# Kernel tuning notes

Measured on AMD Instinct MI355X. Metric: run time of the kernel, lower is better.

The kernel has to match this reference:

```python
import jax, jax.numpy as jnp
import numpy as np

HEADS, DIM, N = 16, 128, 2048
NEG = -1e9


def setup_inputs() -> dict:
    key = jax.random.key(0)
    ks = jax.random.split(key, 8)
    xavier = lambda k, shape, fan: jax.random.uniform(
        k, shape, jnp.float32, -1.0, 1.0) * np.sqrt(6.0 / fan)
    return {
        "q": jax.random.normal(ks[0], (N, DIM), jnp.float32),
        "k": jax.random.normal(ks[1], (N, DIM), jnp.float32),
        "v": jax.random.normal(ks[2], (N, DIM), jnp.float32),
        "mask": jax.random.randint(ks[3], (N, N), 0, 2) > 0,
        "Q": xavier(ks[4], (HEADS, DIM, DIM), 2 * DIM),
        "K": xavier(ks[5], (HEADS, DIM, DIM), 2 * DIM),
        "V": xavier(ks[6], (HEADS, DIM, DIM), 2 * DIM),
        "last": xavier(ks[7], (HEADS * DIM, DIM), HEADS * DIM + DIM),
    }


def reference(q, k, v, Q, K, V, last, mask):
    # per-head projections: [n, d] x [h, d, d] -> [h, n, d]
    qp = jnp.einsum('nd,hde->hne', q, Q)
    kp = jnp.einsum('nd,hde->hne', k, K)
    vp = jnp.einsum('nd,hde->hne', v, V)
    n = qp.shape[1]
    # NOTE: original computes k @ q^T and scales by sqrt(seq_len) (q.size(1) after projection)
    att = jnp.einsum('hid,hjd->hij', kp, qp)  # [h, n, n]
    fmask = mask.astype(jnp.float32)
    att = att * fmask / jnp.sqrt(jnp.float32(n)) + NEG * (1.0 - fmask)
    att = jax.nn.softmax(att, axis=2)
    out = jnp.einsum('hij,hjd->hid', att, vp)            # [h, n, d]
    out = jnp.transpose(out, (1, 0, 2)).reshape(n, -1)   # n (heads d)
    return out @ last
```

## Files before the change

### kernel.cpp

```cpp
#include <hip/hip_runtime.h>
#include <hip/hip_bf16.h>


#define HN 16
#define NN 2048
#define DD 128

typedef __attribute__((ext_vector_type(8))) short short8;
typedef __attribute__((ext_vector_type(4))) short short4v;
typedef __attribute__((ext_vector_type(4))) float float4v;
typedef __attribute__((ext_vector_type(16))) float f32x16;
typedef __attribute__((ext_vector_type(4))) unsigned int uint4v;

#define CROW(r) ((((r) & 3)) + 8 * ((r) >> 2))

__device__ inline unsigned short f2bf(float f) {
    unsigned int u = __builtin_bit_cast(unsigned int, f);
    unsigned int r = (u + 0x7fffu + ((u >> 16) & 1u)) >> 16;
    return (unsigned short)r;
}

__device__ inline unsigned int cvtpk(float lo, float hi) {
    unsigned int w;
    asm("v_cvt_pk_bf16_f32 %0, %1, %2" : "=v"(w) : "v"(lo), "v"(hi));
    return w;
}

__device__ inline void plswap(unsigned int& x, unsigned int& y) {
#if __has_builtin(__builtin_amdgcn_permlane32_swap)
    typedef int int2v __attribute__((ext_vector_type(2)));
    int2v r = __builtin_amdgcn_permlane32_swap((int)x, (int)y, false, false);
    x = (unsigned int)r[0];
    y = (unsigned int)r[1];
#else
    const unsigned int sx = (unsigned int)__shfl_xor((int)x, 32);
    const unsigned int sy = (unsigned int)__shfl_xor((int)y, 32);
    const bool hiHalf = (threadIdx.x & 32) != 0;
    const unsigned int nx = hiHalf ? sy : x;
    const unsigned int ny = hiHalf ? y : sx;
    x = nx; y = ny;
#endif
}

__device__ inline short8 ld_bf8(const float* __restrict__ p) {
    const float4v a = *(const float4v*)p;
    const float4v b = *(const float4v*)(p + 4);
    short8 r;
    r[0] = (short)f2bf(a[0]); r[1] = (short)f2bf(a[1]);
    r[2] = (short)f2bf(a[2]); r[3] = (short)f2bf(a[3]);
    r[4] = (short)f2bf(b[0]); r[5] = (short)f2bf(b[1]);
    r[6] = (short)f2bf(b[2]); r[7] = (short)f2bf(b[3]);
    return r;
}

__device__ inline short8 ld2x4(const unsigned short* p) {
    const short4v lo = *(const short4v*)p;
    const short4v hi = *(const short4v*)(p + 4);
    short8 r;
    r[0] = lo[0]; r[1] = lo[1]; r[2] = lo[2]; r[3] = lo[3];
    r[4] = hi[0]; r[5] = hi[1]; r[6] = hi[2]; r[7] = hi[3];
    return r;
}

__global__ void sentinel_kernel(float* out, int n) {
    int i = blockIdx.x * 256 + threadIdx.x;
    if (i < n) out[i] = 2.0f;
}

__global__ __launch_bounds__(256) void prep_kernel(
    const int* __restrict__ mask,
    unsigned long long* __restrict__ mbT,
    float* __restrict__ out, int out_n,
    const float* __restrict__ Qw,
    const float* __restrict__ Kw,
    const float* __restrict__ Vw,
    unsigned short* __restrict__ wsW)
{
    __shared__ __align__(16) unsigned short Wt[128 * 132];
    const int bx = blockIdx.x;
    const int tid = threadIdx.x;

    if (bx < 4096) {
        const int wgrp = bx * 4 + (tid >> 6);
        const int lane = tid & 63;
        const int word0 = wgrp * 4;
        const int i = word0 >> 5;
        const int w = word0 & 31;
        const int* row = mask + (size_t)i * NN + w * 64;
        unsigned long long b[4];
#pragma unroll
        for (int c = 0; c < 4; c++)
            b[c] = __ballot(row[c * 64 + lane] != 0);
        if (lane == 0) {
#pragma unroll
            for (int c = 0; c < 4; c++) mbT[(size_t)(w + c) * NN + i] = b[c];
        }
        const int z = bx * 256 + tid;
        if (z < out_n) out[z] = 0.f;
    } else {
        const int idx = bx - 4096;
        const int h = idx & 15, t = idx >> 4;
        const float* W = ((t == 0) ? Qw : ((t == 1) ? Kw : Vw)) + h * DD * DD;
        unsigned short* o = wsW + ((size_t)t * HN + h) * DD * DD;

        for (int idx2 = tid * 2; idx2 < DD * DD; idx2 += 512) {
            const int d = idx2 >> 7, e = idx2 & 127;
            const float2 w2 = *(const float2*)(W + idx2);
            Wt[(e + 0) * 132 + d] = f2bf(w2.x);
            Wt[(e + 1) * 132 + d] = f2bf(w2.y);
        }
        __syncthreads();
        for (int idx8 = tid * 8; idx8 < DD * DD; idx8 += 2048) {
            const int e = idx8 >> 7, d = idx8 & 127;
            *(short8*)(o + idx8) = ld2x4(&Wt[e * 132 + d]);
        }
    }
}

__global__ __launch_bounds__(256) void proj4_kernel(
    const float* __restrict__ q,
    const float* __restrict__ k,
    const float* __restrict__ v,
    const unsigned short* __restrict__ wsW,
    unsigned short* __restrict__ ws)
{
    __shared__ __align__(16) unsigned short Wt[128 * 136];
    const int t = blockIdx.z, h = blockIdx.y, cb = blockIdx.x;
    const int tid = threadIdx.x;
    const float* in = (t == 0) ? q : ((t == 1) ? k : v);
    const unsigned short* WTg = wsW + ((size_t)t * HN + h) * DD * DD;
    unsigned short* out = ws + (size_t)t * (HN * NN * DD) + (size_t)h * (NN * DD);

#pragma unroll
    for (int it = 0; it < 8; it++) {
        const int idx8 = tid * 8 + it * 2048;
        const int row = idx8 >> 7, col = idx8 & 127;
        *(short8*)(&Wt[row * 136 + col]) = *(const short8*)(WTg + idx8);
    }
    __syncthreads();

    const int wave = tid >> 6, lane = tid & 63;
    const int quad = lane >> 4, l16 = lane & 15;

#pragma unroll 1
    for (int rt = 0; rt < 2; rt++) {
        const int row0 = cb * 128 + rt * 64 + wave * 16;

        float4v acc[8];
#pragma unroll
        for (int c = 0; c < 8; c++) acc[c] = {0.f, 0.f, 0.f, 0.f};

        if (t < 2) {
#pragma unroll
            for (int kk = 0; kk < 4; kk++) {
                const short8 a = ld_bf8(in + (size_t)(row0 + l16) * DD + kk * 32 + quad * 8);
#pragma unroll
                for (int c = 0; c < 8; c++) {
                    const short8 b = *(const short8*)(&Wt[(c * 16 + l16) * 136 + kk * 32 + quad * 8]);
                    acc[c] = __builtin_amdgcn_mfma_f32_16x16x32_bf16(a, b, acc[c], 0, 0, 0);
                }
            }
            if (t == 0) {
#pragma unroll
                for (int c = 0; c < 8; c++)
#pragma unroll
                    for (int r = 0; r < 4; r++) {
                        const int row = row0 + quad * 4 + r;
                        out[(size_t)(((row >> 5) * 8 + c)) * 512 + (row & 31) * 16 + l16]
                            = f2bf(acc[c][r]);
                    }
            } else {
#pragma unroll
                for (int c = 0; c < 8; c++)
#pragma unroll
                    for (int r = 0; r < 4; r++)
                        out[(size_t)(row0 + quad * 4 + r) * DD + c * 16 + l16] = f2bf(acc[c][r]);
            }
        } else {
#pragma unroll
            for (int kk = 0; kk < 4; kk++) {
                const short8 bv = ld_bf8(in + (size_t)(row0 + l16) * DD + kk * 32 + quad * 8);
#pragma unroll
                for (int c = 0; c < 8; c++) {
                    const short8 aw = *(const short8*)(&Wt[(c * 16 + l16) * 136 + kk * 32 + quad * 8]);
                    acc[c] = __builtin_amdgcn_mfma_f32_16x16x32_bf16(aw, bv, acc[c], 0, 0, 0);
                }
            }
#pragma unroll
            for (int c = 0; c < 8; c++)
#pragma unroll
                for (int r = 0; r < 4; r++) {
                    const int d = c * 16 + quad * 4 + r;
                    out[(size_t)(row0 >> 4) * 2048 + d * 16 + l16] = f2bf(acc[c][r]);
                }
        }
    }
}

__global__ __launch_bounds__(256, 2) void attn_kernel(
    unsigned short* __restrict__ ws,
    const unsigned long long* __restrict__ mbT,
    const float* __restrict__ last,
    float* __restrict__ outp)
{
    __shared__ __align__(16) float obuf[2 * 128 * 33];
    __shared__ __align__(16) unsigned short lastT[128 * 132];
    __shared__ float lbuf[192];

    const int bid = blockIdx.x;
    const int xcd = bid & 7;
    const int h  = xcd + 8 * (bid >> 8);
    const int ib = (bid >> 3) & 31;
    const int tid = threadIdx.x;
    const int wave = tid >> 6, lane = tid & 63;
    const int ig = wave >> 1;
    const int h2 = wave & 1;
    const int l31 = lane & 31;
    const int hi = lane >> 5;

    const unsigned short* qA  = ws + (size_t)h * (NN * DD);
    const unsigned short* kp  = ws + (size_t)(HN * NN * DD) + (size_t)h * (NN * DD);
    const unsigned short* vpB = ws + (size_t)(2 * HN * NN * DD) + (size_t)h * (NN * DD);

    const int i0 = ib * 64;
    const float scale = 0.022097086912079612f;

    {
        const float* lastH = last + (size_t)h * DD * DD;
        for (int idx2 = tid * 2; idx2 < DD * DD; idx2 += 512) {
            const int kk = idx2 >> 7, e = idx2 & 127;
            const float2 w2 = *(const float2*)(lastH + idx2);
            lastT[(e + 0) * 132 + kk] = f2bf(w2.x);
            lastT[(e + 1) * 132 + kk] = f2bf(w2.y);
        }
    }

    short8 kpf[8];
    {
        const int row = i0 + ig * 32 + l31;
#pragma unroll
        for (int kk = 0; kk < 8; kk++)
            kpf[kk] = *(const short8*)(kp + (size_t)row * DD + kk * 16 + hi * 8);
    }

    const unsigned short* qbase = qA + l31 * 16 + hi * 8;
    const unsigned short* vbase = vpB + l31 * 16 + hi * 8;

    f32x16 o[4];
#pragma unroll
    for (int dt = 0; dt < 4; dt++)
#pragma unroll
        for (int r = 0; r < 16; r++) o[dt][r] = 0.f;
    float lacc = 0.f;

    short8 qfA[8], qfB[8];

#define QLD(QF, JT) do {                                                        \
        const unsigned short* p_ = qbase + (size_t)(((JT) * 2 + h2) * 8) * 512; \
        _Pragma("unroll")                                                       \
        for (int kk = 0; kk < 8; kk++)                                          \
            QF[kk] = *(const short8*)(p_ + kk * 512);                           \
    } while (0)

    auto COMPUTE = [&](const short8 (&qf)[8], int jt) {
        short8 vf[8];
#pragma unroll
        for (int ks = 0; ks < 2; ks++)
#pragma unroll
            for (int dt = 0; dt < 4; dt++)
                vf[ks * 4 + dt] = *(const short8*)(vbase
                    + (size_t)(jt * 4 + h2 * 2 + ks) * 2048 + dt * 512);
        const unsigned long long mrow = mbT[(size_t)jt * NN + i0 + ig * 32 + l31];
        const unsigned int m2 = (unsigned int)(mrow >> (h2 * 32 + hi * 4));

        f32x16 s;
#pragma unroll
        for (int r = 0; r < 16; r++) s[r] = 0.f;
        __builtin_amdgcn_s_setprio(1);
#pragma unroll
        for (int kk = 0; kk < 8; kk++)
            s = __builtin_amdgcn_mfma_f32_32x32x16_bf16(qf[kk], kpf[kk], s, 0, 0, 0);
        __builtin_amdgcn_s_setprio(0);

#pragma unroll
        for (int r = 0; r < 16; r++) {
            const float x = ((m2 >> CROW(r)) & 1u) ? fmaf(s[r], scale, -5.0f) : -50.0f;
            s[r] = __expf(x);
        }
        float ls = (((s[0] + s[1]) + (s[2] + s[3])) + ((s[4] + s[5]) + (s[6] + s[7])))
                 + (((s[8] + s[9]) + (s[10] + s[11])) + ((s[12] + s[13]) + (s[14] + s[15])));
        ls += __shfl_xor(ls, 32);
        lacc += ls;

        short8 pa[2];
#pragma unroll
        for (int ks = 0; ks < 2; ks++) {
            const int b = ks * 8;
            unsigned int x0 = cvtpk(s[b + 0], s[b + 1]);
            unsigned int y0 = cvtpk(s[b + 4], s[b + 5]);
            unsigned int x1 = cvtpk(s[b + 2], s[b + 3]);
            unsigned int y1 = cvtpk(s[b + 6], s[b + 7]);
            plswap(x0, y0);
            plswap(x1, y1);
            uint4v w; w[0] = x0; w[1] = x1; w[2] = y0; w[3] = y1;
            pa[ks] = __builtin_bit_cast(short8, w);
        }

        __builtin_amdgcn_s_setprio(1);
#pragma unroll
        for (int ks = 0; ks < 2; ks++)
#pragma unroll
            for (int dt = 0; dt < 4; dt++)
                o[dt] = __builtin_amdgcn_mfma_f32_32x32x16_bf16(pa[ks], vf[ks * 4 + dt], o[dt], 0, 0, 0);
        __builtin_amdgcn_s_setprio(0);
    };

    QLD(qfA, 0);
#pragma unroll 1
    for (int jt = 0; jt < 32; jt += 2) {
        QLD(qfB, jt + 1);
        COMPUTE(qfA, jt);
        if (jt + 2 < 32) QLD(qfA, jt + 2);
        COMPUTE(qfB, jt + 1);
    }
#undef QLD

    if (h2 == 1) {
#pragma unroll
        for (int dt = 0; dt < 4; dt++)
#pragma unroll
            for (int r = 0; r < 16; r++)
                obuf[(size_t)(ig * 128 + dt * 32 + l31) * 33 + CROW(r) + hi * 4] = o[dt][r];
        if (hi == 0) lbuf[ig * 32 + l31] = lacc;
    }
    __syncthreads();

    if (h2 == 0) {
        const float lt = lacc + lbuf[ig * 32 + l31];
        const float inv = (lt > 0.f) ? (1.0f / lt) : 0.f;
        if (hi == 0) lbuf[64 + ig * 32 + l31] = inv;
#pragma unroll
        for (int dt = 0; dt < 4; dt++)
#pragma unroll
            for (int r = 0; r < 16; r++) {
                const int row = CROW(r) + hi * 4;
                const size_t oi = (size_t)(ig * 128 + dt * 32 + l31) * 33 + row;
                obuf[oi] = (o[dt][r] + obuf[oi]) * lbuf[64 + ig * 32 + row];
            }
    }
    __syncthreads();

    short8 af[8];
#pragma unroll
    for (int kk = 0; kk < 8; kk++) {
        const float* ob = &obuf[(size_t)(ig * 128 + kk * 16 + hi * 8) * 33 + l31];
        uint4v w;
        w[0] = cvtpk(ob[0 * 33], ob[1 * 33]);
        w[1] = cvtpk(ob[2 * 33], ob[3 * 33]);
        w[2] = cvtpk(ob[4 * 33], ob[5 * 33]);
        w[3] = cvtpk(ob[6 * 33], ob[7 * 33]);
        af[kk] = __builtin_bit_cast(short8, w);
    }
    f32x16 acc2[2];
#pragma unroll
    for (int ebx = 0; ebx < 2; ebx++)
#pragma unroll
        for (int r = 0; r < 16; r++) acc2[ebx][r] = 0.f;
#pragma unroll
    for (int kk = 0; kk < 8; kk++) {
#pragma unroll
        for (int ebx = 0; ebx < 2; ebx++) {
            const short8 bf = ld2x4(&lastT[(size_t)((h2 * 2 + ebx) * 32 + l31) * 132
                                           + kk * 16 + hi * 8]);
            acc2[ebx] = __builtin_amdgcn_mfma_f32_32x32x16_bf16(af[kk], bf, acc2[ebx], 0, 0, 0);
        }
    }
#pragma unroll
    for (int ebx = 0; ebx < 2; ebx++)
#pragma unroll
        for (int r = 0; r < 16; r++)
            atomicAdd(&outp[(size_t)(i0 + ig * 32 + CROW(r) + 4 * hi) * DD
                            + (h2 * 2 + ebx) * 32 + l31],
                      acc2[ebx][r]);
}

extern "C" void kernel_launch(void* const* d_in, const int* in_sizes, int n_in,
                              void* d_out, int out_size, void* d_ws, size_t ws_size,
                              hipStream_t stream)
{
    const float* q    = (const float*)d_in[0];
    const float* k    = (const float*)d_in[1];
    const float* v    = (const float*)d_in[2];
    const int*   mask = (const int*)d_in[3];
    const float* Qw   = (const float*)d_in[4];
    const float* Kw   = (const float*)d_in[5];
    const float* Vw   = (const float*)d_in[6];
    const float* last = (const float*)d_in[7];
    unsigned short* ws  = (unsigned short*)d_ws;
    float* out = (float*)d_out;

    const size_t shorts_main = (size_t)4 * HN * NN * DD;
    const size_t mb_bytes = (size_t)NN * (NN / 64) * 8;
    const size_t needed = shorts_main * sizeof(unsigned short) + mb_bytes;
    if (ws_size < needed) {
        sentinel_kernel<<<(out_size + 255) / 256, 256, 0, stream>>>(out, out_size);
        return;
    }
    unsigned long long* mbT = (unsigned long long*)(ws + shorts_main);
    unsigned short* wsW = ws + (size_t)3 * HN * NN * DD;

    prep_kernel<<<dim3(4096 + 48), 256, 0, stream>>>(mask, mbT, out, out_size,
                                                     Qw, Kw, Vw, wsW);
    proj4_kernel<<<dim3(16, 16, 3), 256, 0, stream>>>(q, k, v, wsW, ws);
    attn_kernel<<<dim3(512), 256, 0, stream>>>(ws, mbT, last, out);
}
```

Measured before the change: 156.3 us.

## Fuse projection into prep kernel and precompute bf16 output weights

Merges the weight-transpose prep and the per-head Q/K/V projection into one launch: each projection block now converts and transposes its own fp32 weight tile into LDS, so the separate proj kernel and its bf16 weight round trip go away. The mask bit-packing blocks and 16 new blocks that convert the final output weight to bf16 run in the same grid. The attention kernel then loads pre-converted bf16 output weights with vector loads instead of converting fp32 per block. The cost is that each of the 768 projection blocks redoes the fp32 weight conversion, where before it was done once per weight matrix.

```diff
diff --git a/kernel.cpp b/kernel.cpp
--- a/kernel.cpp
+++ b/kernel.cpp
@@ -11,6 +11,7 @@
 typedef __attribute__((ext_vector_type(4))) float float4v;
 typedef __attribute__((ext_vector_type(16))) float f32x16;
 typedef __attribute__((ext_vector_type(4))) unsigned int uint4v;
+typedef __attribute__((ext_vector_type(2))) unsigned int uint2v;
 
 #define CROW(r) ((((r) & 3)) + 8 * ((r) >> 2))
 
@@ -67,21 +68,97 @@
     if (i < n) out[i] = 2.0f;
 }
 
-__global__ __launch_bounds__(256) void prep_kernel(
+__global__ __launch_bounds__(256) void fused_kernel(
+    const float* __restrict__ q,
+    const float* __restrict__ k,
+    const float* __restrict__ v,
     const int* __restrict__ mask,
-    unsigned long long* __restrict__ mbT,
-    float* __restrict__ out, int out_n,
     const float* __restrict__ Qw,
     const float* __restrict__ Kw,
     const float* __restrict__ Vw,
-    unsigned short* __restrict__ wsW)
+    const float* __restrict__ last,
+    unsigned long long* __restrict__ mbT,
+    float* __restrict__ out, int out_n,
+    unsigned short* __restrict__ ws,
+    unsigned short* __restrict__ lastb)
 {
     __shared__ __align__(16) unsigned short Wt[128 * 132];
     const int bx = blockIdx.x;
     const int tid = threadIdx.x;
 
-    if (bx < 4096) {
-        const int wgrp = bx * 4 + (tid >> 6);
+    if (bx < 768) {
+        const int t = bx >> 8, h = (bx >> 4) & 15, cb = bx & 15;
+        const float* in = (t == 0) ? q : ((t == 1) ? k : v);
+        const float* W  = ((t == 0) ? Qw : ((t == 1) ? Kw : Vw)) + h * DD * DD;
+        unsigned short* outp = ws + (size_t)t * (HN * NN * DD) + (size_t)h * (NN * DD);
+
+        for (int idx2 = tid * 2; idx2 < DD * DD; idx2 += 512) {
+            const int d = idx2 >> 7, e = idx2 & 127;
+            const float2 w2 = *(const float2*)(W + idx2);
+            Wt[(e + 0) * 132 + d] = f2bf(w2.x);
+            Wt[(e + 1) * 132 + d] = f2bf(w2.y);
+        }
+        __syncthreads();
+
+        const int wave = tid >> 6, lane = tid & 63;
+        const int quad = lane >> 4, l16 = lane & 15;
+
+#pragma unroll 1
+        for (int rt = 0; rt < 2; rt++) {
+            const int row0 = cb * 128 + rt * 64 + wave * 16;
+
+            float4v acc[8];
+#pragma unroll
+            for (int c = 0; c < 8; c++) acc[c] = {0.f, 0.f, 0.f, 0.f};
+
+            if (t < 2) {
+#pragma unroll
+                for (int kk = 0; kk < 4; kk++) {
+                    const short8 a = ld_bf8(in + (size_t)(row0 + l16) * DD + kk * 32 + quad * 8);
+#pragma unroll
+                    for (int c = 0; c < 8; c++) {
+                        const short8 b = ld2x4(&Wt[(c * 16 + l16) * 132 + kk * 32 + quad * 8]);
+                        acc[c] = __builtin_amdgcn_mfma_f32_16x16x32_bf16(a, b, acc[c], 0, 0, 0);
+                    }
+                }
+                if (t == 0) {
+#pragma unroll
+                    for (int c = 0; c < 8; c++)
+#pragma unroll
+                        for (int r = 0; r < 4; r++) {
+                            const int row = row0 + quad * 4 + r;
+                            outp[(size_t)(((row >> 5) * 8 + c)) * 512 + (row & 31) * 16 + l16]
+                                = f2bf(acc[c][r]);
+                        }
+                } else {
+#pragma unroll
+                    for (int c = 0; c < 8; c++)
+#pragma unroll
+                        for (int r = 0; r < 4; r++)
+                            outp[(size_t)(row0 + quad * 4 + r) * DD + c * 16 + l16] = f2bf(acc[c][r]);
+                }
+            } else {
+#pragma unroll
+                for (int kk = 0; kk < 4; kk++) {
+                    const short8 bv = ld_bf8(in + (size_t)(row0 + l16) * DD + kk * 32 + quad * 8);
+#pragma unroll
+                    for (int c = 0; c < 8; c++) {
+                        const short8 aw = ld2x4(&Wt[(c * 16 + l16) * 132 + kk * 32 + quad * 8]);
+                        acc[c] = __builtin_amdgcn_mfma_f32_16x16x32_bf16(aw, bv, acc[c], 0, 0, 0);
+                    }
+                }
+#pragma unroll
+                for (int c = 0; c < 8; c++)
+#pragma unroll
+                    for (int r = 0; r < 4; r++) {
+                        const int d = c * 16 + quad * 4 + r;
+                        outp[(size_t)(row0 >> 4) * 2048 + d * 16 + l16] = f2bf(acc[c][r]);
+                    }
+            }
+        }
+    } else if (bx < 4864) {
+        const int mbx = bx - 768;
+        const int wgrp = mbx * 4 + (tid >> 6);
         const int lane = tid & 63;
         const int word0 = wgrp * 4;
         const int i = word0 >> 5;
@@ -95,13 +172,12 @@
 #pragma unroll
             for (int c = 0; c < 4; c++) mbT[(size_t)(w + c) * NN + i] = b[c];
         }
-        const int z = bx * 256 + tid;
+        const int z = mbx * 256 + tid;
         if (z < out_n) out[z] = 0.f;
     } else {
-        const int idx = bx - 4096;
-        const int h = idx & 15, t = idx >> 4;
-        const float* W = ((t == 0) ? Qw : ((t == 1) ? Kw : Vw)) + h * DD * DD;
-        unsigned short* o = wsW + ((size_t)t * HN + h) * DD * DD;
+        const int h = bx - 4864;
+        const float* W = last + (size_t)h * DD * DD;
+        unsigned short* o = lastb + (size_t)h * DD * DD;
 
         for (int idx2 = tid * 2; idx2 < DD * DD; idx2 += 512) {
             const int d = idx2 >> 7, e = idx2 & 127;
@@ -117,90 +193,10 @@
     }
 }
 
-__global__ __launch_bounds__(256) void proj4_kernel(
-    const float* __restrict__ q,
-    const float* __restrict__ k,
-    const float* __restrict__ v,
-    const unsigned short* __restrict__ wsW,
-    unsigned short* __restrict__ ws)
-{
-    __shared__ __align__(16) unsigned short Wt[128 * 136];
-    const int t = blockIdx.z, h = blockIdx.y, cb = blockIdx.x;
-    const int tid = threadIdx.x;
-    const float* in = (t == 0) ? q : ((t == 1) ? k : v);
-    const unsigned short* WTg = wsW + ((size_t)t * HN + h) * DD * DD;
-    unsigned short* out = ws + (size_t)t * (HN * NN * DD) + (size_t)h * (NN * DD);
-
-#pragma unroll
-    for (int it = 0; it < 8; it++) {
-        const int idx8 = tid * 8 + it * 2048;
-        const int row = idx8 >> 7, col = idx8 & 127;
-        *(short8*)(&Wt[row * 136 + col]) = *(const short8*)(WTg + idx8);
-    }
-    __syncthreads();
-
-    const int wave = tid >> 6, lane = tid & 63;
-    const int quad = lane >> 4, l16 = lane & 15;
-
-#pragma unroll 1
-    for (int rt = 0; rt < 2; rt++) {
-        const int row0 = cb * 128 + rt * 64 + wave * 16;
-
-        float4v acc[8];
-#pragma unroll
-        for (int c = 0; c < 8; c++) acc[c] = {0.f, 0.f, 0.f, 0.f};
-
-        if (t < 2) {
-#pragma unroll
-            for (int kk = 0; kk < 4; kk++) {
-                const short8 a = ld_bf8(in + (size_t)(row0 + l16) * DD + kk * 32 + quad * 8);
-#pragma unroll
-                for (int c = 0; c < 8; c++) {
-                    const short8 b = *(const short8*)(&Wt[(c * 16 + l16) * 136 + kk * 32 + quad * 8]);
-                    acc[c] = __builtin_amdgcn_mfma_f32_16x16x32_bf16(a, b, acc[c], 0, 0, 0);
-                }
-            }
-            if (t == 0) {
-#pragma unroll
-                for (int c = 0; c < 8; c++)
-#pragma unroll
-                    for (int r = 0; r < 4; r++) {
-                        const int row = row0 + quad * 4 + r;
-                        out[(size_t)(((row >> 5) * 8 + c)) * 512 + (row & 31) * 16 + l16]
-                            = f2bf(acc[c][r]);
-                    }
-            } else {
-#pragma unroll
-                for (int c = 0; c < 8; c++)
-#pragma unroll
-                    for (int r = 0; r < 4; r++)
-                        out[(size_t)(row0 + quad * 4 + r) * DD + c * 16 + l16] = f2bf(acc[c][r]);
-            }
-        } else {
-#pragma unroll
-            for (int kk = 0; kk < 4; kk++) {
-                const short8 bv = ld_bf8(in + (size_t)(row0 + l16) * DD + kk * 32 + quad * 8);
-#pragma unroll
-                for (int c = 0; c < 8; c++) {
-                    const short8 aw = *(const short8*)(&Wt[(c * 16 + l16) * 136 + kk * 32 + quad * 8]);
-                    acc[c] = __builtin_amdgcn_mfma_f32_16x16x32_bf16(aw, bv, acc[c], 0, 0, 0);
-                }
-            }
-#pragma unroll
-            for (int c = 0; c < 8; c++)
-#pragma unroll
-                for (int r = 0; r < 4; r++) {
-                    const int d = c * 16 + quad * 4 + r;
-                    out[(size_t)(row0 >> 4) * 2048 + d * 16 + l16] = f2bf(acc[c][r]);
-                }
-        }
-    }
-}
-
 __global__ __launch_bounds__(256, 2) void attn_kernel(
     unsigned short* __restrict__ ws,
     const unsigned long long* __restrict__ mbT,
-    const float* __restrict__ last,
+    const unsigned short* __restrict__ lastb,
     float* __restrict__ outp)
 {
     __shared__ __align__(16) float obuf[2 * 128 * 33];
@@ -226,12 +222,17 @@
     const float scale = 0.022097086912079612f;
 
     {
-        const float* lastH = last + (size_t)h * DD * DD;
-        for (int idx2 = tid * 2; idx2 < DD * DD; idx2 += 512) {
-            const int kk = idx2 >> 7, e = idx2 & 127;
-            const float2 w2 = *(const float2*)(lastH + idx2);
-            lastT[(e + 0) * 132 + kk] = f2bf(w2.x);
-            lastT[(e + 1) * 132 + kk] = f2bf(w2.y);
+        const unsigned short* lastBh = lastb + (size_t)h * DD * DD;
+#pragma unroll
+        for (int it = 0; it < 8; it++) {
+            const int idx8 = tid * 8 + it * 2048;
+            const int e = idx8 >> 7, kk = idx8 & 127;
+            const short8 x = *(const short8*)(lastBh + idx8);
+            short4v lo, hi4;
+            lo[0] = x[0]; lo[1] = x[1]; lo[2] = x[2]; lo[3] = x[3];
+            hi4[0] = x[4]; hi4[1] = x[5]; hi4[2] = x[6]; hi4[3] = x[7];
+            *(short4v*)(&lastT[e * 132 + kk]) = lo;
+            *(short4v*)(&lastT[e * 132 + kk + 4]) = hi4;
         }
     }
 
@@ -407,10 +408,9 @@
         return;
     }
     unsigned long long* mbT = (unsigned long long*)(ws + shorts_main);
-    unsigned short* wsW = ws + (size_t)3 * HN * NN * DD;
-
-    prep_kernel<<<dim3(4096 + 48), 256, 0, stream>>>(mask, mbT, out, out_size,
-                                                     Qw, Kw, Vw, wsW);
-    proj4_kernel<<<dim3(16, 16, 3), 256, 0, stream>>>(q, k, v, wsW, ws);
-    attn_kernel<<<dim3(512), 256, 0, stream>>>(ws, mbT, last, out);
-}
+    unsigned short* lastb = ws + (size_t)3 * HN * NN * DD;
+
+    fused_kernel<<<dim3(768 + 4096 + 16), 256, 0, stream>>>(
+        q, k, v, mask, Qw, Kw, Vw, last, mbT, out, out_size, ws, lastb);
+    attn_kernel<<<dim3(512), 256, 0, stream>>>(ws, mbT, lastb, out);
+}
```

New measurement: 155.0 us. No clear change (-0.9%).
